# Kernel optimization log

Measured on AMD Instinct MI355X. Metric: run time of the kernel, lower is better.

The kernel has to match this reference:

```python
import jax, jax.numpy as jnp
import numpy as np

HEADS = 8
DIM_HEAD = 64
EPS = 1e-5


def _layernorm(x, g, b):
    m = jnp.mean(x, axis=-1, keepdims=True)
    v = jnp.mean((x - m) ** 2, axis=-1, keepdims=True)
    return (x - m) * jax.lax.rsqrt(v + EPS) * g + b


def setup_inputs() -> dict:
    key = jax.random.key(0)
    ks = jax.random.split(key, 8)
    b, c, hh, ww = 4, 256, 48, 48
    inner = HEADS * DIM_HEAD  # 512
    s = 0.02
    return {
        "x": jax.random.normal(ks[0], (b, c, hh, ww), jnp.float32),
        "Wq": jax.random.normal(ks[1], (c, inner), jnp.float32) * s,
        "Wk": jax.random.normal(ks[2], (c, inner), jnp.float32) * s,
        "Wv": jax.random.normal(ks[3], (c, inner), jnp.float32) * s,
        "Wo": jax.random.normal(ks[4], (inner, c), jnp.float32) * s,
        "bo": jnp.zeros((c,), jnp.float32),
        "g1": jnp.ones((c,), jnp.float32),
        "b1": jnp.zeros((c,), jnp.float32),
        "g2": jnp.ones((c,), jnp.float32),
        "b2": jnp.zeros((c,), jnp.float32),
        "Wf1": jax.random.normal(ks[5], (c, 2 * c), jnp.float32) * s,
        "bf1": jnp.zeros((2 * c,), jnp.float32),
        "Wf2": jax.random.normal(ks[6], (2 * c, c), jnp.float32) * s,
        "bf2": jnp.zeros((c,), jnp.float32),
        "Wp": jax.random.normal(ks[7], (c, c), jnp.float32) * s,
        "bp": jnp.zeros((c,), jnp.float32),
    }


def reference(x, Wq, Wk, Wv, Wo, bo, g1, b1, g2, b2, Wf1, bf1, Wf2, bf2, Wp, bp):
    b, c, hh, ww = x.shape
    n = hh * ww
    scale = DIM_HEAD ** -0.5
    x_in = x
    t = jnp.transpose(x.reshape(b, c, n), (0, 2, 1))  # [b, n, c]

    # --- CrossAttention (self-attn, context=None) ---
    tn = _layernorm(t, g1, b1)
    q = (tn @ Wq).reshape(b, n, HEADS, DIM_HEAD)
    k = (tn @ Wk).reshape(b, n, HEADS, DIM_HEAD)
    v = (tn @ Wv).reshape(b, n, HEADS, DIM_HEAD)
    sim = jnp.einsum("bihd,bjhd->bhij", q, k) * scale  # [b,h,n,n]
    attn = jax.nn.softmax(sim, axis=-1)
    o = jnp.einsum("bhij,bjhd->bihd", attn, v).reshape(b, n, HEADS * DIM_HEAD)
    t = o @ Wo + bo + t

    # --- FeedForward: Linear -> GELU(exact) -> Linear ---
    f = jax.nn.gelu(_layernorm(t, g2, b2) @ Wf1 + bf1, approximate=False)
    t = f @ Wf2 + bf2 + t

    # back to image and 1x1 conv (Wp[c_in, c_out])
    xi = jnp.transpose(t, (0, 2, 1)).reshape(b, c, hh, ww)
    y = jnp.einsum("bchw,co->bohw", xi, Wp) + bp[None, :, None, None]
    return y + x_in
```

## Files before the change

kernel.cpp:

```cpp
#include <hip/hip_runtime.h>
#include <math.h>

#define B_    4
#define C_    256
#define N_    2304
#define H_    8
#define DH_   64
#define IN_   512
#define ROWS_ 9216
#define NHALF 576

typedef __attribute__((ext_vector_type(8))) short short8;
typedef __attribute__((ext_vector_type(4))) float f32x4;
typedef __attribute__((ext_vector_type(16))) float f32x16;

__device__ __forceinline__ unsigned short f2bf(float f) {
    unsigned int u = __float_as_uint(f);
    u += 0x7fffu + ((u >> 16) & 1u);
    return (unsigned short)(u >> 16);
}

__device__ __forceinline__ float bf2f(unsigned short u) {
    return __uint_as_float(((unsigned)u) << 16);
}

__device__ __forceinline__ float gelu_exact(float x) {
    return 0.5f * x * (1.0f + erff(x * 0.70710678118654752440f));
}

__device__ __forceinline__ unsigned cvtpk(float lo, float hi) {
    unsigned r;
    asm("v_cvt_pk_bf16_f32 %0, %1, %2" : "=v"(r) : "v"(lo), "v"(hi));
    return r;
}

__device__ __forceinline__ void gload_lds16(const void* g, void* l) {
    __builtin_amdgcn_global_load_lds(
        (const __attribute__((address_space(1))) unsigned int*)g,
        (__attribute__((address_space(3))) unsigned int*)l, 16, 0, 0);
}

__device__ __forceinline__ const short8* frg(const short* base, int row, int chunk) {
    return (const short8*)(base + (row << 6) + (((chunk) ^ (row & 7)) << 3));
}

__device__ __forceinline__ int swz2(int row) {
    return (row & 7) ^ ((row >> 3) & 3);
}
__device__ __forceinline__ const short8* frg2(const short* base, int row, int chunk) {
    return (const short8*)(base + (row << 6) + (((chunk) ^ swz2(row)) << 3));
}

__global__ __launch_bounds__(256)
void k_pre(const float* __restrict__ Wq, const float* __restrict__ Wk,
           const float* __restrict__ Wv, const float* __restrict__ Wo,
           const float* __restrict__ Wf1, const float* __restrict__ Wf2,
           const float* __restrict__ Wp,
           unsigned short* Wqh, unsigned short* Wkh, unsigned short* Wvh,
           unsigned short* Woh, unsigned short* Wf1h, unsigned short* Wf2h,
           unsigned short* Wph,
           const float* __restrict__ x, float* __restrict__ T,
           unsigned short* __restrict__ TNh,
           const float* __restrict__ g1, const float* __restrict__ b1) {
    __shared__ float tile[32][257];
    int bid = blockIdx.x;
    int tid = threadIdx.x;
    if (bid < 1792) {
        int wz = bid >> 8;
        int rem = bid & 255;
        int nBase = (rem & 15) * 32;
        int kBase = (rem >> 4) * 32;
        const float* src; unsigned short* dst; int K, N;
        switch (wz) {
            case 0: src = Wq;  dst = Wqh;  K = 256; N = 512; break;
            case 1: src = Wk;  dst = Wkh;  K = 256; N = 512; break;
            case 2: src = Wv;  dst = Wvh;  K = 256; N = 512; break;
            case 3: src = Wo;  dst = Woh;  K = 512; N = 256; break;
            case 4: src = Wf1; dst = Wf1h; K = 256; N = 512; break;
            case 5: src = Wf2; dst = Wf2h; K = 512; N = 256; break;
            default: src = Wp; dst = Wph;  K = 256; N = 256; break;
        }
        if (nBase >= N || kBase >= K) return;
        float scl = (wz == 0) ? 0.18033688f : 1.0f;
        int tx = tid & 31, ty = tid >> 5;
        #pragma unroll
        for (int i = 0; i < 32; i += 8)
            tile[ty + i][tx] = src[(size_t)(kBase + ty + i) * N + nBase + tx];
        __syncthreads();
        #pragma unroll
        for (int i = 0; i < 32; i += 8)
            dst[(size_t)(nBase + ty + i) * K + kBase + tx] = f2bf(tile[tx][ty + i] * scl);
    } else {
        int idx = bid - 1792;
        int bb = idx / 72;
        int nBase = (idx - bb * 72) * 32;
        int tx = tid & 31;
        int tg = tid >> 5;
        const float* xp = x + (size_t)bb * C_ * N_ + nBase + tx;
        #pragma unroll
        for (int i = 0; i < 32; ++i) {
            int c = tg * 32 + i;
            tile[tx][c] = xp[(size_t)c * N_];
        }
        __syncthreads();
        int w = tid >> 6, lane = tid & 63;
        float g0 = g1[lane], ga = g1[lane + 64], gb2 = g1[lane + 128], gc = g1[lane + 192];
        float b0 = b1[lane], ba = b1[lane + 64], bb2 = b1[lane + 128], bc = b1[lane + 192];
        #pragma unroll
        for (int r8 = 0; r8 < 8; ++r8) {
            int row = w * 8 + r8;
            float v0 = tile[row][lane],       v1 = tile[row][lane + 64];
            float v2 = tile[row][lane + 128], v3 = tile[row][lane + 192];
            float s = v0 + v1 + v2 + v3;
            #pragma unroll
            for (int m = 1; m < 64; m <<= 1) s += __shfl_xor(s, m);
            float mean = s * (1.0f / C_);
            float d0 = v0 - mean, d1 = v1 - mean, d2 = v2 - mean, d3 = v3 - mean;
            float s2 = d0 * d0 + d1 * d1 + d2 * d2 + d3 * d3;
            #pragma unroll
            for (int m = 1; m < 64; m <<= 1) s2 += __shfl_xor(s2, m);
            float rs = rsqrtf(s2 * (1.0f / C_) + 1e-5f);
            size_t o = (size_t)(bb * N_ + nBase + row) * C_ + lane;
            T[o]       = v0; T[o + 64]  = v1; T[o + 128] = v2; T[o + 192] = v3;
            TNh[o]       = f2bf(d0 * rs * g0 + b0);
            TNh[o + 64]  = f2bf(d1 * rs * ga + ba);
            TNh[o + 128] = f2bf(d2 * rs * gb2 + bb2);
            TNh[o + 192] = f2bf(d3 * rs * gc + bc);
        }
    }
}

__global__ __launch_bounds__(256)
void k_layernorm_bf16(const float* __restrict__ in, unsigned short* __restrict__ out,
                      const float* __restrict__ g, const float* __restrict__ b) {
    int wv = threadIdx.x >> 6;
    int lane = threadIdx.x & 63;
    int row = blockIdx.x * 4 + wv;
    float4 v = ((const float4*)(in + (size_t)row * C_))[lane];
    float s = v.x + v.y + v.z + v.w;
    #pragma unroll
    for (int m = 1; m < 64; m <<= 1) s += __shfl_xor(s, m);
    float mean = s * (1.0f / C_);
    float dx = v.x - mean, dy = v.y - mean, dz = v.z - mean, dw = v.w - mean;
    float s2 = dx * dx + dy * dy + dz * dz + dw * dw;
    #pragma unroll
    for (int m = 1; m < 64; m <<= 1) s2 += __shfl_xor(s2, m);
    float rs = rsqrtf(s2 * (1.0f / C_) + 1e-5f);
    float4 gv = ((const float4*)g)[lane];
    float4 bv = ((const float4*)b)[lane];
    ushort4 o;
    o.x = f2bf(dx * rs * gv.x + bv.x);
    o.y = f2bf(dy * rs * gv.y + bv.y);
    o.z = f2bf(dz * rs * gv.z + bv.z);
    o.w = f2bf(dw * rs * gv.w + bv.w);
    *(ushort4*)(out + (size_t)row * C_ + lane * 4) = o;
}

template <int EP>
__global__ __launch_bounds__(256)
void k_gemm64(const short* __restrict__ A, const short* __restrict__ Bt,
              void* __restrict__ Out, const float* __restrict__ bias,
              const float* __restrict__ Res, int M, int N, int K) {
    __shared__ __align__(16) short As[64 * 64];
    __shared__ __align__(16) short Bs[64 * 64];
    int tid = threadIdx.x;
    int w = tid >> 6;
    int lane = tid & 63;
    int l15 = lane & 15;
    int lg = lane >> 4;
    int wr = w >> 1, wc = w & 1;
    int rowBase = blockIdx.y * 64;
    int colBase = blockIdx.x * 64;

    f32x4 acc[2][2];
    #pragma unroll
    for (int m = 0; m < 2; ++m)
        #pragma unroll
        for (int n = 0; n < 2; ++n) acc[m][n] = (f32x4){0.f, 0.f, 0.f, 0.f};

    for (int k0 = 0; k0 < K; k0 += 64) {
        __syncthreads();
        #pragma unroll
        for (int a = 0; a < 2; ++a) {
            int rr = (w << 4) + (a << 3) + (lane >> 3);
            int cc = (lane & 7) ^ (lane >> 3);
            gload_lds16(A + (size_t)(rowBase + rr) * K + k0 + cc * 8,
                        As + (((w << 4) + (a << 3)) << 6));
            gload_lds16(Bt + (size_t)(colBase + rr) * K + k0 + cc * 8,
                        Bs + (((w << 4) + (a << 3)) << 6));
        }
        asm volatile("s_waitcnt vmcnt(0)" ::: "memory");
        __syncthreads();
        short8 af[2][2], bf[2][2];
        #pragma unroll
        for (int m = 0; m < 2; ++m) {
            af[m][0] = *frg(As, wr * 32 + m * 16 + l15, lg);
            af[m][1] = *frg(As, wr * 32 + m * 16 + l15, 4 + lg);
        }
        #pragma unroll
        for (int n = 0; n < 2; ++n) {
            bf[n][0] = *frg(Bs, wc * 32 + n * 16 + l15, lg);
            bf[n][1] = *frg(Bs, wc * 32 + n * 16 + l15, 4 + lg);
        }
        #pragma unroll
        for (int m = 0; m < 2; ++m)
            #pragma unroll
            for (int n = 0; n < 2; ++n) {
                acc[m][n] = __builtin_amdgcn_mfma_f32_16x16x32_bf16(af[m][0], bf[n][0], acc[m][n], 0, 0, 0);
                acc[m][n] = __builtin_amdgcn_mfma_f32_16x16x32_bf16(af[m][1], bf[n][1], acc[m][n], 0, 0, 0);
            }
    }

    int arB = rowBase + wr * 32;
    int brB = colBase + wc * 32;
    int bb = 0;
    if (EP == 5) bb = brB / N_;
    #pragma unroll
    for (int m = 0; m < 2; ++m) {
        #pragma unroll
        for (int i = 0; i < 4; ++i) {
            int ar = arB + m * 16 + lg * 4 + i;
            #pragma unroll
            for (int n = 0; n < 2; ++n) {
                int br = brB + n * 16 + l15;
                float v = acc[m][n][i];
                if constexpr (EP == 2) {
                    size_t o = (size_t)ar * N + br;
                    ((float*)Out)[o] = v + bias[br] + Res[o];
                } else if constexpr (EP == 3) {
                    ((unsigned short*)Out)[(size_t)ar * N + br] = f2bf(gelu_exact(v + bias[br]));
                } else if constexpr (EP == 4) {
                    size_t o = (size_t)ar * N + br;
                    ((unsigned short*)Out)[o] = f2bf(v + bias[br] + Res[o]);
                } else {
                    size_t o = ((size_t)(bb * C_) + ar) * N_ + (br - bb * N_);
                    ((float*)Out)[o] = v + bias[ar] + Res[o];
                }
            }
        }
    }
}

__global__ __launch_bounds__(256)
void k_gemm_qkv(const short* __restrict__ TNh, const short* __restrict__ Wqh,
                const short* __restrict__ Wkh, const short* __restrict__ Wvh,
                unsigned short* __restrict__ Qb, unsigned short* __restrict__ Kb,
                unsigned short* __restrict__ Vt) {
    __shared__ __align__(16) short As[64 * 64];
    __shared__ __align__(16) short Bs[64 * 64];
    int bid = blockIdx.x;
    int z = bid / 1152;
    int rem = bid - z * 1152;
    int tid = threadIdx.x;
    int w = tid >> 6;
    int lane = tid & 63;
    int l15 = lane & 15;
    int lg = lane >> 4;
    int wr = w >> 1, wc = w & 1;
    const short *A, *Bt;
    int rowBase, colBase;
    if (z < 2) {
        A = TNh; Bt = z ? Wkh : Wqh;
        colBase = (rem & 7) * 64;
        rowBase = (rem >> 3) * 64;
    } else {
        A = Wvh; Bt = TNh;
        colBase = (rem % 144) * 64;
        rowBase = (rem / 144) * 64;
    }
    const int K = C_;

    f32x4 acc[2][2];
    #pragma unroll
    for (int m = 0; m < 2; ++m)
        #pragma unroll
        for (int n = 0; n < 2; ++n) acc[m][n] = (f32x4){0.f, 0.f, 0.f, 0.f};

    for (int k0 = 0; k0 < K; k0 += 64) {
        __syncthreads();
        #pragma unroll
        for (int a = 0; a < 2; ++a) {
            int rr = (w << 4) + (a << 3) + (lane >> 3);
            int cc = (lane & 7) ^ (lane >> 3);
            gload_lds16(A + (size_t)(rowBase + rr) * K + k0 + cc * 8,
                        As + (((w << 4) + (a << 3)) << 6));
            gload_lds16(Bt + (size_t)(colBase + rr) * K + k0 + cc * 8,
                        Bs + (((w << 4) + (a << 3)) << 6));
        }
        asm volatile("s_waitcnt vmcnt(0)" ::: "memory");
        __syncthreads();
        short8 af[2][2], bf[2][2];
        #pragma unroll
        for (int m = 0; m < 2; ++m) {
            af[m][0] = *frg(As, wr * 32 + m * 16 + l15, lg);
            af[m][1] = *frg(As, wr * 32 + m * 16 + l15, 4 + lg);
        }
        #pragma unroll
        for (int n = 0; n < 2; ++n) {
            bf[n][0] = *frg(Bs, wc * 32 + n * 16 + l15, lg);
            bf[n][1] = *frg(Bs, wc * 32 + n * 16 + l15, 4 + lg);
        }
        #pragma unroll
        for (int m = 0; m < 2; ++m)
            #pragma unroll
            for (int n = 0; n < 2; ++n) {
                acc[m][n] = __builtin_amdgcn_mfma_f32_16x16x32_bf16(af[m][0], bf[n][0], acc[m][n], 0, 0, 0);
                acc[m][n] = __builtin_amdgcn_mfma_f32_16x16x32_bf16(af[m][1], bf[n][1], acc[m][n], 0, 0, 0);
            }
    }

    int arB = rowBase + wr * 32;
    int brB = colBase + wc * 32;
    if (z < 2) {
        unsigned short* Out = z ? Kb : Qb;
        #pragma unroll
        for (int m = 0; m < 2; ++m)
            #pragma unroll
            for (int i = 0; i < 4; ++i) {
                int ar = arB + m * 16 + lg * 4 + i;
                #pragma unroll
                for (int n = 0; n < 2; ++n)
                    Out[(size_t)ar * IN_ + brB + n * 16 + l15] = f2bf(acc[m][n][i]);
            }
    } else {
        int bb = brB / N_;
        #pragma unroll
        for (int m = 0; m < 2; ++m)
            #pragma unroll
            for (int i = 0; i < 4; ++i) {
                int ar = arB + m * 16 + lg * 4 + i;
                #pragma unroll
                for (int n = 0; n < 2; ++n) {
                    int br = brB + n * 16 + l15;
                    Vt[((size_t)(bb * IN_) + ar) * N_ + (br - bb * N_)] = f2bf(acc[m][n][i]);
                }
            }
    }
}

__global__ __launch_bounds__(256)
void k_flash_mfma(const short* __restrict__ Qb, const short* __restrict__ Kb,
                  const short* __restrict__ Vt,
                  unsigned short* O0, unsigned short* O1,
                  unsigned short* O2, unsigned short* O3,
                  float* __restrict__ Lsum) {
    __shared__ __align__(16) short Ks[64 * 64];
    __shared__ __align__(16) short Vs[64 * 64];
    int tid = threadIdx.x;
    int lane = tid & 63;
    int l31 = lane & 31;
    int h5 = lane >> 5;
    int w = tid >> 6;

    int logical = (blockIdx.x & 7) * 288 + (blockIdx.x >> 3);
    int pair = logical / 18;
    int qi = logical - pair * 18;
    int bh = pair & 31;
    int half = pair >> 5;
    int bb = bh >> 3, h = bh & 7;
    int qBase = qi * 128;
    int h0 = half * NHALF;

    const short* Qp = Qb + ((size_t)bb * N_ + qBase + w * 32) * IN_ + h * DH_;
    const short* Kp = Kb + (size_t)bb * N_ * IN_ + h * DH_;
    const short* Vp = Vt + ((size_t)bb * IN_ + h * DH_) * N_;

    short8 qf[4];
    #pragma unroll
    for (int kk = 0; kk < 4; ++kk)
        qf[kk] = *(const short8*)(Qp + (size_t)l31 * IN_ + kk * 16 + h5 * 8);

    short8 ones;
    #pragma unroll
    for (int j = 0; j < 8; ++j) ones[j] = (short)0x3F80;

    int r0s = tid >> 3, c0s = tid & 7;
    int r1s = (tid + 256) >> 3, c1s = tid & 7;
    int w0s = (c0s ^ swz2(r0s)) << 3;
    int w1s = (c1s ^ swz2(r1s)) << 3;
    uint4 kreg0 = *(const uint4*)(Kp + (size_t)(h0 + r0s) * IN_ + c0s * 8);
    uint4 kreg1 = *(const uint4*)(Kp + (size_t)(h0 + r1s) * IN_ + c1s * 8);
    uint4 vreg0 = *(const uint4*)(Vp + (size_t)r0s * N_ + h0 + c0s * 8);
    uint4 vreg1 = *(const uint4*)(Vp + (size_t)r1s * N_ + h0 + c1s * 8);

    f32x16 oacc0 = (f32x16)(0.0f);
    f32x16 oacc1 = (f32x16)(0.0f);
    f32x16 lacc  = (f32x16)(0.0f);

    for (int kt = h0; kt < h0 + NHALF; kt += 64) {
        __syncthreads();
        *(uint4*)(Ks + (r0s << 6) + w0s) = kreg0;
        *(uint4*)(Ks + (r1s << 6) + w1s) = kreg1;
        *(uint4*)(Vs + (r0s << 6) + w0s) = vreg0;
        *(uint4*)(Vs + (r1s << 6) + w1s) = vreg1;
        __syncthreads();
        if (kt + 64 < h0 + NHALF) {
            kreg0 = *(const uint4*)(Kp + (size_t)(kt + 64 + r0s) * IN_ + c0s * 8);
            kreg1 = *(const uint4*)(Kp + (size_t)(kt + 64 + r1s) * IN_ + c1s * 8);
            vreg0 = *(const uint4*)(Vp + (size_t)r0s * N_ + kt + 64 + c0s * 8);
            vreg1 = *(const uint4*)(Vp + (size_t)r1s * N_ + kt + 64 + c1s * 8);
        }

        short8 pa[4];
        #pragma unroll
        for (int s = 0; s < 2; ++s) {
            f32x16 stv = (f32x16)(0.0f);
            __builtin_amdgcn_s_setprio(1);
            #pragma unroll
            for (int kk = 0; kk < 4; ++kk) {
                short8 kf = *frg2(Ks, s * 32 + l31, kk * 2 + h5);
                stv = __builtin_amdgcn_mfma_f32_32x32x16_bf16(kf, qf[kk], stv, 0, 0, 0);
            }
            __builtin_amdgcn_s_setprio(0);
            unsigned u[8];
            #pragma unroll
            for (int q = 0; q < 4; ++q) {
                u[2 * q]     = cvtpk(exp2f(stv[4 * q + 0]), exp2f(stv[4 * q + 1]));
                u[2 * q + 1] = cvtpk(exp2f(stv[4 * q + 2]), exp2f(stv[4 * q + 3]));
            }
            asm volatile("v_permlane32_swap_b32 %0, %1" : "+v"(u[0]), "+v"(u[2]));
            asm volatile("v_permlane32_swap_b32 %0, %1" : "+v"(u[1]), "+v"(u[3]));
            asm volatile("v_permlane32_swap_b32 %0, %1" : "+v"(u[4]), "+v"(u[6]));
            asm volatile("v_permlane32_swap_b32 %0, %1" : "+v"(u[5]), "+v"(u[7]));
            union { unsigned uu[4]; short8 s8; } c0, c1;
            c0.uu[0] = u[0]; c0.uu[1] = u[1]; c0.uu[2] = u[2]; c0.uu[3] = u[3];
            c1.uu[0] = u[4]; c1.uu[1] = u[5]; c1.uu[2] = u[6]; c1.uu[3] = u[7];
            pa[2 * s]     = c0.s8;
            pa[2 * s + 1] = c1.s8;
        }

        __builtin_amdgcn_s_setprio(1);
        #pragma unroll
        for (int kk = 0; kk < 4; ++kk) {
            short8 vf0 = *frg2(Vs, l31, kk * 2 + h5);
            short8 vf1 = *frg2(Vs, 32 + l31, kk * 2 + h5);
            lacc  = __builtin_amdgcn_mfma_f32_32x32x16_bf16(pa[kk], ones, lacc, 0, 0, 0);
            oacc0 = __builtin_amdgcn_mfma_f32_32x32x16_bf16(pa[kk], vf0, oacc0, 0, 0, 0);
            oacc1 = __builtin_amdgcn_mfma_f32_32x32x16_bf16(pa[kk], vf1, oacc1, 0, 0, 0);
        }
        __builtin_amdgcn_s_setprio(0);
    }

    unsigned short* OpH = (half == 0) ? O0 : (half == 1) ? O1 : (half == 2) ? O2 : O3;
    unsigned short* Op = OpH + ((size_t)bb * N_ + qBase + w * 32) * IN_ + h * DH_;
    #pragma unroll
    for (int reg = 0; reg < 16; ++reg) {
        int q = (reg & 3) + 8 * (reg >> 2) + 4 * h5;
        Op[(size_t)q * IN_ + l31]      = f2bf(oacc0[reg]);
        Op[(size_t)q * IN_ + 32 + l31] = f2bf(oacc1[reg]);
    }
    if (l31 == 0) {
        float* Lp = Lsum + (((size_t)half * B_ + bb) * H_ + h) * N_ + qBase + w * 32;
        #pragma unroll
        for (int reg = 0; reg < 16; ++reg) {
            int q = (reg & 3) + 8 * (reg >> 2) + 4 * h5;
            Lp[q] = lacc[reg];
        }
    }
}

__global__ __launch_bounds__(256)
void k_combine(const unsigned short* p0, const unsigned short* p1,
               const unsigned short* p2, const unsigned short* p3,
               const float* __restrict__ Lsum, unsigned short* Ob) {
    int wv = threadIdx.x >> 6;
    int lane = threadIdx.x & 63;
    int row = blockIdx.x * 4 + wv;
    int bb = row / N_;
    int n = row - bb * N_;
    int hh = lane >> 3;
    float l = 0.f;
    #pragma unroll
    for (int q4 = 0; q4 < 4; ++q4)
        l += Lsum[(((size_t)q4 * B_ + bb) * H_ + hh) * N_ + n];
    float inv = 1.0f / l;
    size_t off = (size_t)row * IN_ + lane * 8;
    short8 a0 = *(const short8*)(p0 + off);
    short8 a1 = *(const short8*)(p1 + off);
    short8 a2 = *(const short8*)(p2 + off);
    short8 a3 = *(const short8*)(p3 + off);
    unsigned short o[8];
    #pragma unroll
    for (int j = 0; j < 8; ++j)
        o[j] = f2bf((bf2f((unsigned short)a0[j]) + bf2f((unsigned short)a1[j]) +
                     bf2f((unsigned short)a2[j]) + bf2f((unsigned short)a3[j])) * inv);
    *(uint4*)(Ob + off) = *(uint4*)o;
}

extern "C" void kernel_launch(void* const* d_in, const int* in_sizes, int n_in,
                              void* d_out, int out_size, void* d_ws, size_t ws_size,
                              hipStream_t stream) {
    (void)in_sizes; (void)n_in; (void)out_size; (void)ws_size;
    const float* x   = (const float*)d_in[0];
    const float* Wq  = (const float*)d_in[1];
    const float* Wk  = (const float*)d_in[2];
    const float* Wv  = (const float*)d_in[3];
    const float* Wo  = (const float*)d_in[4];
    const float* bo  = (const float*)d_in[5];
    const float* g1  = (const float*)d_in[6];
    const float* b1  = (const float*)d_in[7];
    const float* g2  = (const float*)d_in[8];
    const float* b2  = (const float*)d_in[9];
    const float* Wf1 = (const float*)d_in[10];
    const float* bf1 = (const float*)d_in[11];
    const float* Wf2 = (const float*)d_in[12];
    const float* bf2 = (const float*)d_in[13];
    const float* Wp  = (const float*)d_in[14];
    const float* bp  = (const float*)d_in[15];
    float* out = (float*)d_out;
    float* ws  = (float*)d_ws;

    float* T    = ws;
    float* T2   = ws + 2359296;
    unsigned short* TNh = (unsigned short*)(ws + 4718592);
    short* Qb   = (short*)(ws + 5898240);
    short* Kb   = (short*)(ws + 8257536);
    short* Vt   = (short*)(ws + 10616832);
    unsigned short* Obh = (unsigned short*)(ws + 12976128);
    short* F    = (short*)(ws + 15335424);
    short* T3h  = (short*)(ws + 17694720);
    unsigned short* Wqh  = (unsigned short*)(ws + 18874368);
    unsigned short* Wkh  = (unsigned short*)(ws + 18939904);
    unsigned short* Wvh  = (unsigned short*)(ws + 19005440);
    unsigned short* Woh  = (unsigned short*)(ws + 19070976);
    unsigned short* Wf1h = (unsigned short*)(ws + 19136512);
    unsigned short* Wf2h = (unsigned short*)(ws + 19202048);
    unsigned short* Wph  = (unsigned short*)(ws + 19267584);
    unsigned short* Op0  = (unsigned short*)(ws + 19398656);
    unsigned short* Op3  = (unsigned short*)(ws + 21757952);
    unsigned short* Op1  = Obh;
    unsigned short* Op2  = (unsigned short*)F;
    float* Lsum = ws + 24117248;

    k_pre<<<dim3(2080), 256, 0, stream>>>(Wq, Wk, Wv, Wo, Wf1, Wf2, Wp,
                                          Wqh, Wkh, Wvh, Woh, Wf1h, Wf2h, Wph,
                                          x, T, TNh, g1, b1);
    k_gemm_qkv<<<dim3(3456), 256, 0, stream>>>((const short*)TNh, (const short*)Wqh,
                                               (const short*)Wkh, (const short*)Wvh,
                                               (unsigned short*)Qb, (unsigned short*)Kb,
                                               (unsigned short*)Vt);
    k_flash_mfma<<<dim3(2304), 256, 0, stream>>>(Qb, Kb, Vt, Op0, Op1, Op2, Op3, Lsum);
    k_combine<<<2304, 256, 0, stream>>>(Op0, Op1, Op2, Op3, Lsum, Obh);
    k_gemm64<2><<<dim3(4, 144), 256, 0, stream>>>((const short*)Obh, (const short*)Woh, T2, bo, T, ROWS_, C_, IN_);
    k_layernorm_bf16<<<2304, 256, 0, stream>>>(T2, TNh, g2, b2);
    k_gemm64<3><<<dim3(8, 144), 256, 0, stream>>>((const short*)TNh, (const short*)Wf1h, F, bf1, nullptr, ROWS_, IN_, C_);
    k_gemm64<4><<<dim3(4, 144), 256, 0, stream>>>((const short*)F, (const short*)Wf2h, T3h, bf2, T2, ROWS_, C_, IN_);
    k_gemm64<5><<<dim3(144, 4), 256, 0, stream>>>((const short*)Wph, (const short*)T3h, out, bp, x, C_, ROWS_, C_);
}
```

Before: 155.2 us.

## Fuse split-K attention combine into the Wo projection GEMM A-tile load

Replaces the separate combine kernel, which summed the four partial attention outputs and normalized by the softmax denominator, with a small kernel that only computes inverse row sums. The Wo GEMM now loads the four partials directly, sums and scales them while staging its A tile into shared memory. This removes the write and re-read of the combined bf16 attention output. In exchange, each of the 4 column blocks of the GEMM redoes the combine work and reads four times as much A data.

```diff
diff --git a/kernel.cpp b/kernel.cpp
--- a/kernel.cpp
+++ b/kernel.cpp
@@ -224,10 +224,7 @@
             for (int n = 0; n < 2; ++n) {
                 int br = brB + n * 16 + l15;
                 float v = acc[m][n][i];
-                if constexpr (EP == 2) {
-                    size_t o = (size_t)ar * N + br;
-                    ((float*)Out)[o] = v + bias[br] + Res[o];
-                } else if constexpr (EP == 3) {
+                if constexpr (EP == 3) {
                     ((unsigned short*)Out)[(size_t)ar * N + br] = f2bf(gelu_exact(v + bias[br]));
                 } else if constexpr (EP == 4) {
                     size_t o = (size_t)ar * N + br;
@@ -236,6 +233,94 @@
                     size_t o = ((size_t)(bb * C_) + ar) * N_ + (br - bb * N_);
                     ((float*)Out)[o] = v + bias[ar] + Res[o];
                 }
+            }
+        }
+    }
+}
+
+__global__ __launch_bounds__(256)
+void k_gemm_wo64(const unsigned short* p0, const unsigned short* p1,
+                 const unsigned short* p2, const unsigned short* p3,
+                 const short* __restrict__ Bt, float* __restrict__ Out,
+                 const float* __restrict__ bias, const float* __restrict__ Res,
+                 const float* __restrict__ IL) {
+    __shared__ __align__(16) short As[64 * 64];
+    __shared__ __align__(16) short Bs[64 * 64];
+    const int N = C_, K = IN_;
+    int tid = threadIdx.x;
+    int w = tid >> 6;
+    int lane = tid & 63;
+    int l15 = lane & 15;
+    int lg = lane >> 4;
+    int wr = w >> 1, wc = w & 1;
+    int rowBase = blockIdx.y * 64;
+    int colBase = blockIdx.x * 64;
+    int bbT = rowBase / N_;
+    int nB  = rowBase - bbT * N_;
+
+    f32x4 acc[2][2];
+    #pragma unroll
+    for (int m = 0; m < 2; ++m)
+        #pragma unroll
+        for (int n = 0; n < 2; ++n) acc[m][n] = (f32x4){0.f, 0.f, 0.f, 0.f};
+
+    for (int k0 = 0; k0 < K; k0 += 64) {
+        int head = k0 >> 6;
+        __syncthreads();
+        #pragma unroll
+        for (int a = 0; a < 2; ++a) {
+            int rr = (w << 4) + (a << 3) + (lane >> 3);
+            int ch = lane & 7;
+            int cc = ch ^ (lane >> 3);
+            gload_lds16(Bt + (size_t)(colBase + rr) * K + k0 + cc * 8,
+                        Bs + (((w << 4) + (a << 3)) << 6));
+            float inv = IL[((size_t)bbT * H_ + head) * N_ + nB + rr];
+            size_t off = (size_t)(rowBase + rr) * IN_ + k0 + ch * 8;
+            short8 a0 = *(const short8*)(p0 + off);
+            short8 a1 = *(const short8*)(p1 + off);
+            short8 a2 = *(const short8*)(p2 + off);
+            short8 a3 = *(const short8*)(p3 + off);
+            union { unsigned short o[8]; uint4 v; } pk;
+            #pragma unroll
+            for (int j = 0; j < 8; ++j)
+                pk.o[j] = f2bf((bf2f((unsigned short)a0[j]) + bf2f((unsigned short)a1[j]) +
+                                bf2f((unsigned short)a2[j]) + bf2f((unsigned short)a3[j])) * inv);
+            *(uint4*)(As + (rr << 6) + ((ch ^ (rr & 7)) << 3)) = pk.v;
+        }
+        asm volatile("s_waitcnt vmcnt(0)" ::: "memory");
+        __syncthreads();
+        short8 af[2][2], bf[2][2];
+        #pragma unroll
+        for (int m = 0; m < 2; ++m) {
+            af[m][0] = *frg(As, wr * 32 + m * 16 + l15, lg);
+            af[m][1] = *frg(As, wr * 32 + m * 16 + l15, 4 + lg);
+        }
+        #pragma unroll
+        for (int n = 0; n < 2; ++n) {
+            bf[n][0] = *frg(Bs, wc * 32 + n * 16 + l15, lg);
+            bf[n][1] = *frg(Bs, wc * 32 + n * 16 + l15, 4 + lg);
+        }
+        #pragma unroll
+        for (int m = 0; m < 2; ++m)
+            #pragma unroll
+            for (int n = 0; n < 2; ++n) {
+                acc[m][n] = __builtin_amdgcn_mfma_f32_16x16x32_bf16(af[m][0], bf[n][0], acc[m][n], 0, 0, 0);
+                acc[m][n] = __builtin_amdgcn_mfma_f32_16x16x32_bf16(af[m][1], bf[n][1], acc[m][n], 0, 0, 0);
+            }
+    }
+
+    int arB = rowBase + wr * 32;
+    int brB = colBase + wc * 32;
+    #pragma unroll
+    for (int m = 0; m < 2; ++m) {
+        #pragma unroll
+        for (int i = 0; i < 4; ++i) {
+            int ar = arB + m * 16 + lg * 4 + i;
+            #pragma unroll
+            for (int n = 0; n < 2; ++n) {
+                int br = brB + n * 16 + l15;
+                size_t o = (size_t)ar * N + br;
+                Out[o] = acc[m][n][i] + bias[br] + Res[o];
             }
         }
     }
@@ -460,31 +545,18 @@
 }
 
 __global__ __launch_bounds__(256)
-void k_combine(const unsigned short* p0, const unsigned short* p1,
-               const unsigned short* p2, const unsigned short* p3,
-               const float* __restrict__ Lsum, unsigned short* Ob) {
-    int wv = threadIdx.x >> 6;
-    int lane = threadIdx.x & 63;
-    int row = blockIdx.x * 4 + wv;
-    int bb = row / N_;
-    int n = row - bb * N_;
-    int hh = lane >> 3;
-    float l = 0.f;
-    #pragma unroll
-    for (int q4 = 0; q4 < 4; ++q4)
-        l += Lsum[(((size_t)q4 * B_ + bb) * H_ + hh) * N_ + n];
-    float inv = 1.0f / l;
-    size_t off = (size_t)row * IN_ + lane * 8;
-    short8 a0 = *(const short8*)(p0 + off);
-    short8 a1 = *(const short8*)(p1 + off);
-    short8 a2 = *(const short8*)(p2 + off);
-    short8 a3 = *(const short8*)(p3 + off);
-    unsigned short o[8];
-    #pragma unroll
-    for (int j = 0; j < 8; ++j)
-        o[j] = f2bf((bf2f((unsigned short)a0[j]) + bf2f((unsigned short)a1[j]) +
-                     bf2f((unsigned short)a2[j]) + bf2f((unsigned short)a3[j])) * inv);
-    *(uint4*)(Ob + off) = *(uint4*)o;
+void k_invl(const float* __restrict__ Lsum, float* __restrict__ IL) {
+    int i = (blockIdx.x * 256 + threadIdx.x) * 4;
+    float4 a = *(const float4*)(Lsum + i);
+    float4 b = *(const float4*)(Lsum + 73728 + i);
+    float4 c = *(const float4*)(Lsum + 147456 + i);
+    float4 d = *(const float4*)(Lsum + 221184 + i);
+    float4 o;
+    o.x = 1.0f / (a.x + b.x + c.x + d.x);
+    o.y = 1.0f / (a.y + b.y + c.y + d.y);
+    o.z = 1.0f / (a.z + b.z + c.z + d.z);
+    o.w = 1.0f / (a.w + b.w + c.w + d.w);
+    *(float4*)(IL + i) = o;
 }
 
 extern "C" void kernel_launch(void* const* d_in, const int* in_sizes, int n_in,
@@ -516,7 +588,7 @@
     short* Qb   = (short*)(ws + 5898240);
     short* Kb   = (short*)(ws + 8257536);
     short* Vt   = (short*)(ws + 10616832);
-    unsigned short* Obh = (unsigned short*)(ws + 12976128);
+    unsigned short* Op1 = (unsigned short*)(ws + 12976128);
     short* F    = (short*)(ws + 15335424);
     short* T3h  = (short*)(ws + 17694720);
     unsigned short* Wqh  = (unsigned short*)(ws + 18874368);
@@ -528,9 +600,9 @@
     unsigned short* Wph  = (unsigned short*)(ws + 19267584);
     unsigned short* Op0  = (unsigned short*)(ws + 19398656);
     unsigned short* Op3  = (unsigned short*)(ws + 21757952);
-    unsigned short* Op1  = Obh;
     unsigned short* Op2  = (unsigned short*)F;
     float* Lsum = ws + 24117248;
+    float* IL   = (float*)T3h;
 
     k_pre<<<dim3(2080), 256, 0, stream>>>(Wq, Wk, Wv, Wo, Wf1, Wf2, Wp,
                                           Wqh, Wkh, Wvh, Woh, Wf1h, Wf2h, Wph,
@@ -540,8 +612,9 @@
                                                (unsigned short*)Qb, (unsigned short*)Kb,
                                                (unsigned short*)Vt);
     k_flash_mfma<<<dim3(2304), 256, 0, stream>>>(Qb, Kb, Vt, Op0, Op1, Op2, Op3, Lsum);
-    k_combine<<<2304, 256, 0, stream>>>(Op0, Op1, Op2, Op3, Lsum, Obh);
-    k_gemm64<2><<<dim3(4, 144), 256, 0, stream>>>((const short*)Obh, (const short*)Woh, T2, bo, T, ROWS_, C_, IN_);
+    k_invl<<<dim3(72), 256, 0, stream>>>(Lsum, IL);
+    k_gemm_wo64<<<dim3(4, 144), 256, 0, stream>>>(Op0, Op1, Op2, Op3, (const short*)Woh,
+                                                  T2, bo, T, IL);
     k_layernorm_bf16<<<2304, 256, 0, stream>>>(T2, TNh, g2, b2);
     k_gemm64<3><<<dim3(8, 144), 256, 0, stream>>>((const short*)TNh, (const short*)Wf1h, F, bf1, nullptr, ROWS_, IN_, C_);
     k_gemm64<4><<<dim3(4, 144), 256, 0, stream>>>((const short*)F, (const short*)Wf2h, T3h, bf2, T2, ROWS_, C_, IN_);
```

Measured after the change: 163.7 us. +5.4%, slower.
